# Kernel optimization log

Hardware: AMD Instinct MI355X
Metric: run time of the kernel (lower is better)

## Reference

```python
import math
import jax, jax.numpy as jnp
import numpy as np

B, FEAT, H, W = 4, 256, 48, 48
NH = 8
PE = 10            # pe_dim -> 3*PE = 30 positional channels
DK = FEAT // NH    # 32
DV = FEAT // NH    # 32
SCALE = 2.0 * math.pi
TEMPERATURE = 10000.0
BN_EPS = 1e-5


def pos_en_sine(h, w, num_pos_feats=PE):
    """3-axis sine positional encoding (y, x, and a constant 'o' axis) -> [3*PE, h, w]."""
    eps = 1e-6
    ones = jnp.ones((h, w), jnp.float32)
    y_embed = jnp.cumsum(ones, axis=0)
    x_embed = jnp.cumsum(ones, axis=1)
    y_embed = y_embed / (y_embed[-1:, :] + eps) * SCALE
    x_embed = x_embed / (x_embed[:, -1:] + eps) * SCALE
    o_embed = ones * SCALE  # third axis, constant when no explicit pos is given
    dim_t = jnp.arange(num_pos_feats, dtype=jnp.float32)
    dim_t = TEMPERATURE ** (2.0 * jnp.floor(dim_t / 2.0) / num_pos_feats)

    def enc(e):  # e: [h, w] -> [h, w, PE] interleaved sin/cos
        p = e[..., None] / dim_t
        return jnp.stack([jnp.sin(p[..., 0::2]), jnp.cos(p[..., 1::2])], axis=-1).reshape(h, w, num_pos_feats)

    pe = jnp.concatenate([enc(y_embed), enc(x_embed), enc(o_embed)], axis=-1)  # [h, w, 3*PE]
    return jnp.transpose(pe, (2, 0, 1))  # [3*PE, h, w]


def conv1x1(w, x):  # w: [out_c, in_c], x: [b, in_c, h, w]
    return jnp.einsum('oc,bchw->bohw', w, x)


def setup_inputs() -> dict:
    key = jax.random.key(0)
    ks = jax.random.split(key, 16)
    s = 0.02
    return {
        'q': jax.random.normal(ks[0], (B, FEAT, H, W), jnp.float32),
        'k': jax.random.normal(ks[1], (B, FEAT, H, W), jnp.float32),
        'v': jax.random.normal(ks[2], (B, FEAT, H, W), jnp.float32),
        'wq': jax.random.normal(ks[3], (NH * DK, FEAT + 3 * PE), jnp.float32) * s,
        'wk': jax.random.normal(ks[4], (NH * DK, FEAT + 3 * PE), jnp.float32) * s,
        'wv': jax.random.normal(ks[5], (NH * DV, FEAT), jnp.float32) * s,
        'wfc': jax.random.normal(ks[6], (FEAT, NH * DV), jnp.float32) * s,
        'w1': jax.random.normal(ks[7], (FEAT, FEAT), jnp.float32) * s,
        'b1': jnp.zeros((FEAT,), jnp.float32),
        'w2': jax.random.normal(ks[8], (FEAT, FEAT), jnp.float32) * s,
        'b2': jnp.zeros((FEAT,), jnp.float32),
        'gamma': jnp.ones((FEAT,), jnp.float32),
        'beta': jnp.zeros((FEAT,), jnp.float32),
    }


def reference(q, k, v, wq, wk, wv, wfc, w1, b1, w2, b2, gamma, beta):
    b, c, h, w = q.shape
    n = h * w
    pe = pos_en_sine(h, w)                                # [3*PE, h, w]
    peb = jnp.broadcast_to(pe[None], (b,) + pe.shape)
    qc = jnp.concatenate([q, peb], axis=1)                # [b, FEAT+30, h, w]
    kc = jnp.concatenate([k, peb], axis=1)
    # multi-head softmax attention over all spatial tokens
    Q = conv1x1(wq, qc).reshape(b, NH, DK, n)             # [b, nh, dk, n]
    K = conv1x1(wk, kc).reshape(b, NH, DK, n)
    V = conv1x1(wv, v).reshape(b, NH, DV, n)
    scores = jnp.einsum('bhdn,bhdm->bhnm', Q, K) / jnp.sqrt(jnp.float32(DK))
    attn = jax.nn.softmax(scores, axis=-1)                # [b, nh, n, n]
    O = jnp.einsum('bhnm,bhdm->bhdn', attn, V).reshape(b, NH * DV, h, w)
    O = conv1x1(wfc, O)                                   # [b, FEAT, h, w]
    # pointwise FFN + residual
    h1 = jax.nn.relu(conv1x1(w1, O) + b1[None, :, None, None])
    h2 = conv1x1(w2, h1) + b2[None, :, None, None]
    out = O + h2
    # BatchNorm2d (training mode: batch statistics over (b, h, w), biased var)
    mean = jnp.mean(out, axis=(0, 2, 3), keepdims=True)
    var = jnp.var(out, axis=(0, 2, 3), keepdims=True)
    out = (out - mean) / jnp.sqrt(var + BN_EPS)
    out = out * gamma[None, :, None, None] + beta[None, :, None, None]
    return out
```

## Files before the change

### kernel.cpp

```cpp
#include <hip/hip_runtime.h>
#include <hip/hip_bf16.h>

#define NTOK 2304

typedef short  short8  __attribute__((ext_vector_type(8)));
typedef unsigned short ushort8v __attribute__((ext_vector_type(8)));
typedef float  f32x4   __attribute__((ext_vector_type(4)));

static __device__ __forceinline__ unsigned short f2bfu(float f){
  __hip_bfloat16 h = __float2bfloat16(f);
  union { __hip_bfloat16 h; unsigned short u; } cv; cv.h = h; return cv.u;
}

static __device__ __forceinline__ void plane32(unsigned &a, unsigned &b){
  asm("v_permlane32_swap_b32 %0, %1" : "+v"(a), "+v"(b));
}
static __device__ __forceinline__ void plane16(unsigned &a, unsigned &b){
  asm("v_permlane16_swap_b32 %0, %1" : "+v"(a), "+v"(b));
}
static __device__ __forceinline__ short8 xpose_p(f32x4 sa, f32x4 sb){
  unsigned x0, x1, y0, y1;
  asm("v_cvt_pk_bf16_f32 %0, %1, %2" : "=v"(x0) : "v"(sa[0]), "v"(sa[1]));
  asm("v_cvt_pk_bf16_f32 %0, %1, %2" : "=v"(x1) : "v"(sa[2]), "v"(sa[3]));
  asm("v_cvt_pk_bf16_f32 %0, %1, %2" : "=v"(y0) : "v"(sb[0]), "v"(sb[1]));
  asm("v_cvt_pk_bf16_f32 %0, %1, %2" : "=v"(y1) : "v"(sb[2]), "v"(sb[3]));
  plane32(x0, y0);
  plane32(x1, y1);
  plane16(x0, y0);
  plane16(x1, y1);
  union { unsigned u[4]; short8 s; } r;
  r.u[0] = x0; r.u[1] = x1; r.u[2] = y0; r.u[3] = y1;
  return r.s;
}


__global__ void trip_kernel(float* out, int n){
  int i = blockIdx.x*256 + threadIdx.x;
  if (i < n) out[i] = 1000.0f;
}

__global__ __launch_bounds__(256) void setup_kernel(
    const float* __restrict__ q, const float* __restrict__ k,
    const float* __restrict__ v,
    const float* __restrict__ wq, const float* __restrict__ wk,
    const float* __restrict__ wv, const float* __restrict__ wfc,
    const float* __restrict__ w1, const float* __restrict__ w2,
    unsigned short* __restrict__ qT, unsigned short* __restrict__ kT,
    unsigned short* __restrict__ vT,
    unsigned short* __restrict__ wqp, unsigned short* __restrict__ wkp,
    unsigned short* __restrict__ wvb, unsigned short* __restrict__ wfcb,
    unsigned short* __restrict__ w1b, unsigned short* __restrict__ w2b,
    float* __restrict__ bns){
  const int bid = blockIdx.x;
  const int t = threadIdx.x;
  __shared__ __align__(16) unsigned short tile[64*72];

  if (bid < 1728){
    if (bid == 0){ bns[t] = 0.f; bns[256+t] = 0.f; }
    const int x = bid % 36, rem = bid / 36;
    const int y = rem % 4, z = rem / 4;
    const int tz = z >> 2, b = z & 3;
    const float* src = (tz==0) ? q : ((tz==1) ? k : v);
    unsigned short* dst = (tz==0) ? qT : ((tz==1) ? kT : vT);
    const int W = (tz==2) ? 256 : 288;
    const int n0 = x*64, c0 = y*64;
    const int jj = t & 7, cl = t >> 3;
    #pragma unroll
    for (int p=0; p<2; p++){
      int c = c0 + 32*p + cl;
      const float* s = src + (size_t)(b*256 + c)*NTOK + n0 + 8*jj;
      float4 f0 = *(const float4*)s;
      float4 f1 = *(const float4*)(s + 4);
      unsigned short* tr = tile + 32*p + cl;
      tr[(8*jj+0)*72] = f2bfu(f0.x); tr[(8*jj+1)*72] = f2bfu(f0.y);
      tr[(8*jj+2)*72] = f2bfu(f0.z); tr[(8*jj+3)*72] = f2bfu(f0.w);
      tr[(8*jj+4)*72] = f2bfu(f1.x); tr[(8*jj+5)*72] = f2bfu(f1.y);
      tr[(8*jj+6)*72] = f2bfu(f1.z); tr[(8*jj+7)*72] = f2bfu(f1.w);
    }
    __syncthreads();
    #pragma unroll
    for (int p=0; p<2; p++){
      int nl = 32*p + cl;
      ushort8v val = *(const ushort8v*)(tile + nl*72 + 8*jj);
      *(ushort8v*)(dst + (size_t)(b*2304 + n0 + nl)*W + c0 + 8*jj) = val;
    }
  } else if (bid < 1800){
    const int id2 = bid - 1728;
    const int x = id2 % 9, yy = id2 / 9;
    const int n = x*256 + t;
    unsigned short* buf = (yy < 4) ? qT : kT;
    const int b = yy & 3;
    const int i = n / 48, j = n - 48*i;
    const float k2pi = 6.283185307179586f;
    const float f = k2pi / 48.000001f;
    float ey = (float)(i+1) * f;
    float ex = (float)(j+1) * f;
    unsigned short u[32];
    #pragma unroll
    for (int p=0; p<10; p++){
      float inv = exp2f(-2.6575424759098898f * (float)(p >> 1));
      float vy = ey*inv, vx = ex*inv, vo = k2pi*inv;
      u[p]    = f2bfu((p&1) ? cosf(vy) : sinf(vy));
      u[10+p] = f2bfu((p&1) ? cosf(vx) : sinf(vx));
      u[20+p] = f2bfu((p&1) ? cosf(vo) : sinf(vo));
    }
    u[30] = 0; u[31] = 0;
    unsigned short* dst = buf + (size_t)(b*2304 + n)*288 + 256;
    #pragma unroll
    for (int m=0; m<4; m++) *(ushort8v*)(dst + 8*m) = *(const ushort8v*)(u + 8*m);
  } else if (bid < 2376){
    const int id3 = bid - 1800;
    const int x = id3 % 288, y = id3 / 288;
    const int idx = x*256 + t;
    const float* src = y ? wk : wq;
    unsigned short* dst = y ? wkp : wqp;
    const float scale = y ? 1.f : 0.25503486f;
    int row = idx / 288, col = idx - row*288;
    dst[idx] = (col < 286) ? f2bfu(src[row*286 + col] * scale) : (unsigned short)0;
  } else {
    const int id4 = bid - 2376;
    const int x = id4 % 256, y = id4 / 256;
    const int idx = x*256 + t;
    const float* src = (y==0)?wv:((y==1)?wfc:((y==2)?w1:w2));
    unsigned short* dst = (y==0)?wvb:((y==1)?wfcb:((y==2)?w1b:w2b));
    dst[idx] = f2bfu(src[idx]);
  }
}

template<int KSTEPS>
static __device__ __forceinline__ void gemm3_core(
    const unsigned short* __restrict__ a0,
    const unsigned short* __restrict__ a1,
    const unsigned short* __restrict__ a2,
    const unsigned short* __restrict__ wrow, int wstride, f32x4 acc[3][2]){
  #pragma unroll
  for (int kk=0; kk<KSTEPS; kk++){
    short8 af0 = *(const short8*)(a0 + 32*kk);
    short8 af1 = *(const short8*)(a1 + 32*kk);
    short8 af2 = *(const short8*)(a2 + 32*kk);
    #pragma unroll
    for (int to=0; to<2; to++){
      short8 bf = *(const short8*)(wrow + (size_t)(16*to)*wstride + 32*kk);
      acc[0][to] = __builtin_amdgcn_mfma_f32_16x16x32_bf16(af0, bf, acc[0][to], 0,0,0);
      acc[1][to] = __builtin_amdgcn_mfma_f32_16x16x32_bf16(af1, bf, acc[1][to], 0,0,0);
      acc[2][to] = __builtin_amdgcn_mfma_f32_16x16x32_bf16(af2, bf, acc[2][to], 0,0,0);
    }
  }
}

static __device__ __forceinline__ void epi_tok(
    const f32x4* acc, unsigned short* __restrict__ out_tok,
    int b, int tok, int n0, int lane, int quad, int cc,
    unsigned short* __restrict__ tlw){
  #pragma unroll
  for (int to=0; to<2; to++)
    #pragma unroll
    for (int r=0; r<4; r++)
      tlw[(4*quad + r)*40 + 16*to + cc] = f2bfu(acc[to][r]);
  const int row = lane & 15, ch = lane >> 4;
  ushort8v val = *(const ushort8v*)(tlw + row*40 + 8*ch);
  *(ushort8v*)(out_tok + (size_t)(b*2304 + tok + row)*256 + n0 + 8*ch) = val;
}

static __device__ __forceinline__ void epi_chan(
    const f32x4* acc, unsigned short* __restrict__ out_chan,
    int b, int tok, int n0, int quad, int cc){
  #pragma unroll
  for (int to=0; to<2; to++){
    ushort4 pk;
    pk.x = f2bfu(acc[to][0]); pk.y = f2bfu(acc[to][1]);
    pk.z = f2bfu(acc[to][2]); pk.w = f2bfu(acc[to][3]);
    *(ushort4*)(out_chan + (size_t)(b*256 + n0 + 16*to + cc)*NTOK + tok + 4*quad) = pk;
  }
}

__global__ __launch_bounds__(256) void qkv_kernel(
    const unsigned short* __restrict__ qT, const unsigned short* __restrict__ kT,
    const unsigned short* __restrict__ vT,
    const unsigned short* __restrict__ wqp, const unsigned short* __restrict__ wkp,
    const unsigned short* __restrict__ wvb,
    unsigned short* __restrict__ Qt, unsigned short* __restrict__ Kt,
    unsigned short* __restrict__ V2){
  const int t = threadIdx.x;
  const int w = t >> 6, lane = t & 63;
  const int quad = lane >> 4, cc = lane & 15;
  const int t0 = blockIdx.x*192, n0 = blockIdx.y*32;
  const int tz = blockIdx.z >> 2, b = blockIdx.z & 3;
  const int tok = t0 + 48*w;
  __shared__ __align__(16) unsigned short tl[4*16*40];
  unsigned short* tlw = tl + w*640;

  f32x4 acc[3][2];
  #pragma unroll
  for (int f=0; f<3; f++){
    acc[f][0] = (f32x4){0.f,0.f,0.f,0.f};
    acc[f][1] = acc[f][0];
  }

  if (tz == 0){
    const unsigned short* a0 = qT + (size_t)(b*2304 + tok + cc)*288 + 8*quad;
    gemm3_core<9>(a0, a0 + (size_t)16*288, a0 + (size_t)32*288,
                  wqp + (size_t)(n0 + cc)*288 + 8*quad, 288, acc);
    epi_tok(acc[0], Qt, b, tok,      n0, lane, quad, cc, tlw);
    epi_tok(acc[1], Qt, b, tok + 16, n0, lane, quad, cc, tlw);
    epi_tok(acc[2], Qt, b, tok + 32, n0, lane, quad, cc, tlw);
  } else if (tz == 1){
    const unsigned short* a0 = kT + (size_t)(b*2304 + tok + cc)*288 + 8*quad;
    gemm3_core<9>(a0, a0 + (size_t)16*288, a0 + (size_t)32*288,
                  wkp + (size_t)(n0 + cc)*288 + 8*quad, 288, acc);
    epi_tok(acc[0], Kt, b, tok,      n0, lane, quad, cc, tlw);
    epi_tok(acc[1], Kt, b, tok + 16, n0, lane, quad, cc, tlw);
    epi_tok(acc[2], Kt, b, tok + 32, n0, lane, quad, cc, tlw);
  } else {
    const unsigned short* a0 = vT + (size_t)(b*2304 + tok + cc)*256 + 8*quad;
    gemm3_core<8>(a0, a0 + (size_t)16*256, a0 + (size_t)32*256,
                  wvb + (size_t)(n0 + cc)*256 + 8*quad, 256, acc);
    epi_chan(acc[0], V2, b, tok,      n0, quad, cc);
    epi_chan(acc[1], V2, b, tok + 16, n0, quad, cc);
    epi_chan(acc[2], V2, b, tok + 32, n0, quad, cc);
  }
}

__global__ __launch_bounds__(256) void ffn_kernel(
    const unsigned short* __restrict__ AO,
    const unsigned short* __restrict__ wfcb,
    const unsigned short* __restrict__ w1b,
    const unsigned short* __restrict__ w2b,
    const float* __restrict__ b1, const float* __restrict__ b2,
    float* __restrict__ pre_out, float* __restrict__ bns){
  const int t = threadIdx.x;
  const int w = t >> 6, lane = t & 63;
  const int quad = lane >> 4, cc = lane & 15;
  const int tok0 = blockIdx.x * 16;
  const int b = blockIdx.y;
  const int ocb = 64 * w;

  __shared__ __align__(16) unsigned short T0[16*264];
  __shared__ __align__(16) unsigned short T1[16*264];

  const unsigned short* arow = AO + (size_t)(b*2304 + tok0 + cc)*256 + 8*quad;
  f32x4 acc1[4];
  acc1[0] = (f32x4){0.f,0.f,0.f,0.f}; acc1[1]=acc1[0]; acc1[2]=acc1[0]; acc1[3]=acc1[0];
  #pragma unroll
  for (int kk=0; kk<8; kk++){
    short8 af = *(const short8*)(arow + 32*kk);
    #pragma unroll
    for (int of=0; of<4; of++){
      short8 bf = *(const short8*)(wfcb + (size_t)(ocb + 16*of + cc)*256 + 8*quad + 32*kk);
      acc1[of] = __builtin_amdgcn_mfma_f32_16x16x32_bf16(af, bf, acc1[of], 0,0,0);
    }
  }
  #pragma unroll
  for (int of=0; of<4; of++)
    #pragma unroll
    for (int r=0; r<4; r++)
      T0[(4*quad + r)*264 + ocb + 16*of + cc] = f2bfu(acc1[of][r]);
  __syncthreads();

  f32x4 acc2[4];
  acc2[0] = (f32x4){0.f,0.f,0.f,0.f}; acc2[1]=acc2[0]; acc2[2]=acc2[0]; acc2[3]=acc2[0];
  #pragma unroll
  for (int kk=0; kk<8; kk++){
    short8 af = *(const short8*)(T0 + cc*264 + 8*quad + 32*kk);
    #pragma unroll
    for (int of=0; of<4; of++){
      short8 bf = *(const short8*)(w1b + (size_t)(ocb + 16*of + cc)*256 + 8*quad + 32*kk);
      acc2[of] = __builtin_amdgcn_mfma_f32_16x16x32_bf16(af, bf, acc2[of], 0,0,0);
    }
  }
  #pragma unroll
  for (int of=0; of<4; of++){
    float bv = b1[ocb + 16*of + cc];
    #pragma unroll
    for (int r=0; r<4; r++){
      float hv = fmaxf(acc2[of][r] + bv, 0.f);
      T1[(4*quad + r)*264 + ocb + 16*of + cc] = f2bfu(hv);
    }
  }
  __syncthreads();

  f32x4 acc3[4];
  acc3[0] = (f32x4){0.f,0.f,0.f,0.f}; acc3[1]=acc3[0]; acc3[2]=acc3[0]; acc3[3]=acc3[0];
  #pragma unroll
  for (int kk=0; kk<8; kk++){
    short8 af = *(const short8*)(T1 + cc*264 + 8*quad + 32*kk);
    #pragma unroll
    for (int of=0; of<4; of++){
      short8 bf = *(const short8*)(w2b + (size_t)(ocb + 16*of + cc)*256 + 8*quad + 32*kk);
      acc3[of] = __builtin_amdgcn_mfma_f32_16x16x32_bf16(af, bf, acc3[of], 0,0,0);
    }
  }
  #pragma unroll
  for (int of=0; of<4; of++){
    const int oc = ocb + 16*of + cc;
    float bv = b2[oc];
    float p0 = acc3[of][0] + bv + acc1[of][0];
    float p1 = acc3[of][1] + bv + acc1[of][1];
    float p2 = acc3[of][2] + bv + acc1[of][2];
    float p3 = acc3[of][3] + bv + acc1[of][3];
    *(float4*)(pre_out + (size_t)(b*256 + oc)*NTOK + tok0 + 4*quad) =
        make_float4(p0, p1, p2, p3);
    float s1 = (p0+p1)+(p2+p3);
    float s2 = (p0*p0+p1*p1)+(p2*p2+p3*p3);
    s1 += __shfl_xor(s1, 16, 64); s1 += __shfl_xor(s1, 32, 64);
    s2 += __shfl_xor(s2, 16, 64); s2 += __shfl_xor(s2, 32, 64);
    if (quad == 0){
      atomicAdd(&bns[oc],       s1);
      atomicAdd(&bns[256 + oc], s2);
    }
  }
}

__global__ __launch_bounds__(256) void attn_kernel(
    const unsigned short* __restrict__ Qt, const unsigned short* __restrict__ Kt,
    const unsigned short* __restrict__ V2, unsigned short* __restrict__ AO){
  const int t = threadIdx.x;
  const int w = t >> 6, lane = t & 63;
  const int quad = lane >> 4, cc = lane & 15;
  const int h = blockIdx.y, b = blockIdx.z;
  const int q0 = blockIdx.x*64;

  const unsigned short* qb = Qt + (size_t)(b*2304 + q0 + cc)*256 + h*32 + 8*quad;
  short8 qf0 = *(const short8*)(qb);
  short8 qf1 = *(const short8*)(qb + 16*256);
  short8 qf2 = *(const short8*)(qb + 32*256);
  short8 qf3 = *(const short8*)(qb + 48*256);

  const unsigned short* kb = Kt + (size_t)(b*2304 + cc)*256 + h*32 + 8*quad;
  const unsigned short* vb = V2 + (size_t)(b*256 + h*32 + cc)*NTOK + 8*quad;

  __shared__ __align__(16) float mg_lds[4*1600];

  f32x4 o00={0.f,0.f,0.f,0.f}, o10=o00, o01=o00, o11=o00;
  f32x4 o02=o00, o12=o00, o03=o00, o13=o00;
  float lsum0=0.f, lsum1=0.f, lsum2=0.f, lsum3=0.f;

  const int kstart = w*576;
  short8 kf0 = *(const short8*)(kb + (size_t)kstart*256);
  short8 kf1 = *(const short8*)(kb + (size_t)(kstart+16)*256);
  short8 vf0 = *(const short8*)(vb + kstart);
  short8 vf1 = *(const short8*)(vb + (size_t)16*NTOK + kstart);

  #pragma unroll 1
  for (int it = 0; it < 18; ++it){
    const int ko = kstart + it*32;
    const int rk = (it < 17) ? ko + 32 : kstart;
    const f32x4 z = {0.f,0.f,0.f,0.f};

    f32x4 s00 = __builtin_amdgcn_mfma_f32_16x16x32_bf16(kf0, qf0, z, 0,0,0);
    f32x4 s10 = __builtin_amdgcn_mfma_f32_16x16x32_bf16(kf1, qf0, z, 0,0,0);
    f32x4 s01 = __builtin_amdgcn_mfma_f32_16x16x32_bf16(kf0, qf1, z, 0,0,0);
    f32x4 s11 = __builtin_amdgcn_mfma_f32_16x16x32_bf16(kf1, qf1, z, 0,0,0);
    f32x4 s02 = __builtin_amdgcn_mfma_f32_16x16x32_bf16(kf0, qf2, z, 0,0,0);
    f32x4 s12 = __builtin_amdgcn_mfma_f32_16x16x32_bf16(kf1, qf2, z, 0,0,0);
    f32x4 s03 = __builtin_amdgcn_mfma_f32_16x16x32_bf16(kf0, qf3, z, 0,0,0);
    f32x4 s13 = __builtin_amdgcn_mfma_f32_16x16x32_bf16(kf1, qf3, z, 0,0,0);
    kf0 = *(const short8*)(kb + (size_t)rk*256);
    kf1 = *(const short8*)(kb + (size_t)(rk+16)*256);

    #pragma unroll
    for (int r=0; r<4; r++){
      s00[r] = __builtin_amdgcn_exp2f(s00[r]);
      s10[r] = __builtin_amdgcn_exp2f(s10[r]);
      s01[r] = __builtin_amdgcn_exp2f(s01[r]);
      s11[r] = __builtin_amdgcn_exp2f(s11[r]);
      s02[r] = __builtin_amdgcn_exp2f(s02[r]);
      s12[r] = __builtin_amdgcn_exp2f(s12[r]);
      s03[r] = __builtin_amdgcn_exp2f(s03[r]);
      s13[r] = __builtin_amdgcn_exp2f(s13[r]);
    }
    lsum0 += ((s00[0]+s00[1])+(s00[2]+s00[3])) + ((s10[0]+s10[1])+(s10[2]+s10[3]));
    lsum1 += ((s01[0]+s01[1])+(s01[2]+s01[3])) + ((s11[0]+s11[1])+(s11[2]+s11[3]));
    lsum2 += ((s02[0]+s02[1])+(s02[2]+s02[3])) + ((s12[0]+s12[1])+(s12[2]+s12[3]));
    lsum3 += ((s03[0]+s03[1])+(s03[2]+s03[3])) + ((s13[0]+s13[1])+(s13[2]+s13[3]));

    short8 pf0 = xpose_p(s00, s10);
    short8 pf1 = xpose_p(s01, s11);
    short8 pf2 = xpose_p(s02, s12);
    short8 pf3 = xpose_p(s03, s13);

    o00 = __builtin_amdgcn_mfma_f32_16x16x32_bf16(vf0, pf0, o00, 0,0,0);
    o10 = __builtin_amdgcn_mfma_f32_16x16x32_bf16(vf1, pf0, o10, 0,0,0);
    o01 = __builtin_amdgcn_mfma_f32_16x16x32_bf16(vf0, pf1, o01, 0,0,0);
    o11 = __builtin_amdgcn_mfma_f32_16x16x32_bf16(vf1, pf1, o11, 0,0,0);
    o02 = __builtin_amdgcn_mfma_f32_16x16x32_bf16(vf0, pf2, o02, 0,0,0);
    o12 = __builtin_amdgcn_mfma_f32_16x16x32_bf16(vf1, pf2, o12, 0,0,0);
    o03 = __builtin_amdgcn_mfma_f32_16x16x32_bf16(vf0, pf3, o03, 0,0,0);
    o13 = __builtin_amdgcn_mfma_f32_16x16x32_bf16(vf1, pf3, o13, 0,0,0);
    vf0 = *(const short8*)(vb + rk);
    vf1 = *(const short8*)(vb + (size_t)16*NTOK + rk);
  }

  lsum0 += __shfl_xor(lsum0, 16, 64); lsum0 += __shfl_xor(lsum0, 32, 64);
  lsum1 += __shfl_xor(lsum1, 16, 64); lsum1 += __shfl_xor(lsum1, 32, 64);
  lsum2 += __shfl_xor(lsum2, 16, 64); lsum2 += __shfl_xor(lsum2, 32, 64);
  lsum3 += __shfl_xor(lsum3, 16, 64); lsum3 += __shfl_xor(lsum3, 32, 64);

  float* mg = mg_lds + w*1600;
  #pragma unroll
  for (int qq=0; qq<4; qq++){
    f32x4 a0, a1;
    if (qq==0){ a0=o00; a1=o10; }
    else if (qq==1){ a0=o01; a1=o11; }
    else if (qq==2){ a0=o02; a1=o12; }
    else { a0=o03; a1=o13; }
    if (qq != w){
      const int p = (qq < w) ? qq : qq - 1;
      #pragma unroll
      for (int i=0;i<4;i++){
        mg[(p*8 + i)*64 + lane]     = a0[i];
        mg[(p*8 + 4 + i)*64 + lane] = a1[i];
      }
    }
  }
  if (quad == 0){
    mg[1536 +  0 + cc] = lsum0;
    mg[1536 + 16 + cc] = lsum1;
    mg[1536 + 32 + cc] = lsum2;
    mg[1536 + 48 + cc] = lsum3;
  }
  __syncthreads();

  f32x4 R0, R1; float ls;
  if (w==0){ R0=o00; R1=o10; ls=lsum0; }
  else if (w==1){ R0=o01; R1=o11; ls=lsum1; }
  else if (w==2){ R0=o02; R1=o12; ls=lsum2; }
  else { R0=o03; R1=o13; ls=lsum3; }
  #pragma unroll
  for (int v=0; v<4; v++){
    if (v == w) continue;
    const float* m = mg_lds + v*1600;
    const int p = (w < v) ? w : w - 1;
    #pragma unroll
    for (int i=0;i<4;i++){
      R0[i] += m[(p*8 + i)*64 + lane];
      R1[i] += m[(p*8 + 4 + i)*64 + lane];
    }
    ls += m[1536 + w*16 + cc];
  }
  float inv = 1.f / ls;

  const int qcol = q0 + w*16 + cc;
  unsigned short* dst = AO + (size_t)(b*2304 + qcol)*256 + h*32 + 4*quad;
  ushort4 p0;
  p0.x = f2bfu(R0[0]*inv); p0.y = f2bfu(R0[1]*inv);
  p0.z = f2bfu(R0[2]*inv); p0.w = f2bfu(R0[3]*inv);
  *(ushort4*)(dst) = p0;
  ushort4 p1;
  p1.x = f2bfu(R1[0]*inv); p1.y = f2bfu(R1[1]*inv);
  p1.z = f2bfu(R1[2]*inv); p1.w = f2bfu(R1[3]*inv);
  *(ushort4*)(dst + 16) = p1;
}

__global__ __launch_bounds__(256) void bn_final_kernel(
    const float* __restrict__ pre, const float* __restrict__ bns,
    const float* __restrict__ g, const float* __restrict__ bt,
    float* __restrict__ out){
  int i0 = (blockIdx.x*256 + threadIdx.x)*4;
  int ch = (i0 / NTOK) & 255;
  float mean = bns[ch] * (1.f/9216.f);
  float var  = bns[256+ch] * (1.f/9216.f) - mean*mean;
  float scl = g[ch] * rsqrtf(fmaxf(var, 0.f) + 1e-5f);
  float sh  = bt[ch] - mean*scl;
  float4 x = *(const float4*)(pre + i0);
  *(float4*)(out + i0) = make_float4(x.x*scl+sh, x.y*scl+sh, x.z*scl+sh, x.w*scl+sh);
}

extern "C" void kernel_launch(void* const* d_in, const int* in_sizes, int n_in,
                              void* d_out, int out_size, void* d_ws, size_t ws_size,
                              hipStream_t stream){
  const size_t NEED = 2112 + (size_t)15155200*2;
  if (ws_size < NEED){
    trip_kernel<<<dim3((out_size+255)/256), dim3(256), 0, stream>>>((float*)d_out, out_size);
    return;
  }
  const float* q   = (const float*)d_in[0];
  const float* k   = (const float*)d_in[1];
  const float* v   = (const float*)d_in[2];
  const float* wq  = (const float*)d_in[3];
  const float* wk  = (const float*)d_in[4];
  const float* wv  = (const float*)d_in[5];
  const float* wfc = (const float*)d_in[6];
  const float* w1  = (const float*)d_in[7];
  const float* b1  = (const float*)d_in[8];
  const float* w2  = (const float*)d_in[9];
  const float* b2  = (const float*)d_in[10];
  const float* gm  = (const float*)d_in[11];
  const float* bt  = (const float*)d_in[12];

  float* ws  = (float*)d_ws;
  float* bns = ws;
  unsigned short* ub = (unsigned short*)(ws + 528);
  unsigned short* u_qT = ub;
  unsigned short* u_kT = ub + 2654208;
  unsigned short* u_vT = ub + 5308416;
  unsigned short* u_Qt = ub + 7667712;
  unsigned short* u_Kt = ub + 10027008;
  unsigned short* u_V2 = ub + 12386304;
  unsigned short* wqp  = ub + 14745600;
  unsigned short* wkp  = ub + 14819328;
  unsigned short* wvb  = ub + 14893056;
  unsigned short* wfcb = ub + 14958592;
  unsigned short* w1b  = ub + 15024128;
  unsigned short* w2b  = ub + 15089664;
  unsigned short* AO  = u_qT;
  float* pre = (float*)(u_Kt);

  setup_kernel<<<dim3(3400), dim3(256), 0, stream>>>(
      q, k, v, wq, wk, wv, wfc, w1, w2,
      u_qT, u_kT, u_vT, wqp, wkp, wvb, wfcb, w1b, w2b, bns);

  qkv_kernel<<<dim3(12,8,12), dim3(256), 0, stream>>>(u_qT, u_kT, u_vT, wqp, wkp, wvb, u_Qt, u_Kt, u_V2);

  attn_kernel<<<dim3(36,8,4), dim3(256), 0, stream>>>(u_Qt, u_Kt, u_V2, AO);

  ffn_kernel<<<dim3(144,4), dim3(256), 0, stream>>>(AO, wfcb, w1b, w2b, b1, b2, pre, bns);

  bn_final_kernel<<<dim3(2304), dim3(256), 0, stream>>>(pre, bns, gm, bt, (float*)d_out);
}
```

Before: 220.8 us.

## Fuse BatchNorm finalization into FFN kernel via grid-wide atomic barrier

Removes the separate bn_final kernel and the fp32 pre-normalization intermediate buffer. Each FFN block keeps its results in registers, increments a global counter and spins until all 576 blocks have contributed their channel statistics. It then reads the reduced sums and writes normalized output directly. This saves a full write and read of the activation tensor plus one launch. The cost is a spin barrier that only works if every block is co-resident, which should hold for 576 blocks on this GPU.

```diff
diff --git a/kernel.cpp b/kernel.cpp
--- a/kernel.cpp
+++ b/kernel.cpp
@@ -56,7 +56,10 @@
   __shared__ __align__(16) unsigned short tile[64*72];
 
   if (bid < 1728){
-    if (bid == 0){ bns[t] = 0.f; bns[256+t] = 0.f; }
+    if (bid == 0){
+      bns[t] = 0.f; bns[256+t] = 0.f;
+      if (t == 0) *(unsigned*)(bns + 512) = 0u;
+    }
     const int x = bid % 36, rem = bid / 36;
     const int y = rem % 4, z = rem / 4;
     const int tz = z >> 2, b = z & 3;
@@ -227,7 +230,9 @@
     const unsigned short* __restrict__ w1b,
     const unsigned short* __restrict__ w2b,
     const float* __restrict__ b1, const float* __restrict__ b2,
-    float* __restrict__ pre_out, float* __restrict__ bns){
+    const float* __restrict__ gm, const float* __restrict__ bt,
+    float* __restrict__ out, float* __restrict__ bns,
+    unsigned* __restrict__ ctr){
   const int t = threadIdx.x;
   const int w = t >> 6, lane = t & 63;
   const int quad = lane >> 4, cc = lane & 15;
@@ -298,8 +303,6 @@
     float p1 = acc3[of][1] + bv + acc1[of][1];
     float p2 = acc3[of][2] + bv + acc1[of][2];
     float p3 = acc3[of][3] + bv + acc1[of][3];
-    *(float4*)(pre_out + (size_t)(b*256 + oc)*NTOK + tok0 + 4*quad) =
-        make_float4(p0, p1, p2, p3);
     float s1 = (p0+p1)+(p2+p3);
     float s2 = (p0*p0+p1*p1)+(p2*p2+p3*p3);
     s1 += __shfl_xor(s1, 16, 64); s1 += __shfl_xor(s1, 32, 64);
@@ -308,6 +311,33 @@
       atomicAdd(&bns[oc],       s1);
       atomicAdd(&bns[256 + oc], s2);
     }
+  }
+
+  __threadfence();
+  __syncthreads();
+  if (t == 0){
+    atomicAdd(ctr, 1u);
+    const unsigned nb = gridDim.x * gridDim.y;
+    while (atomicAdd(ctr, 0u) < nb){ __builtin_amdgcn_s_sleep(2); }
+  }
+  __syncthreads();
+
+  #pragma unroll
+  for (int of=0; of<4; of++){
+    const int oc = ocb + 16*of + cc;
+    float sA = atomicAdd(&bns[oc],       0.f);
+    float sB = atomicAdd(&bns[256 + oc], 0.f);
+    float mean = sA * (1.f/9216.f);
+    float var  = sB * (1.f/9216.f) - mean*mean;
+    float scl = gm[oc] * rsqrtf(fmaxf(var, 0.f) + 1e-5f);
+    float sh  = bt[oc] - mean*scl;
+    float bv = b2[oc];
+    float p0 = acc3[of][0] + bv + acc1[of][0];
+    float p1 = acc3[of][1] + bv + acc1[of][1];
+    float p2 = acc3[of][2] + bv + acc1[of][2];
+    float p3 = acc3[of][3] + bv + acc1[of][3];
+    *(float4*)(out + (size_t)(b*256 + oc)*NTOK + tok0 + 4*quad) =
+        make_float4(p0*scl+sh, p1*scl+sh, p2*scl+sh, p3*scl+sh);
   }
 }
 
@@ -452,20 +482,6 @@
   *(ushort4*)(dst + 16) = p1;
 }
 
-__global__ __launch_bounds__(256) void bn_final_kernel(
-    const float* __restrict__ pre, const float* __restrict__ bns,
-    const float* __restrict__ g, const float* __restrict__ bt,
-    float* __restrict__ out){
-  int i0 = (blockIdx.x*256 + threadIdx.x)*4;
-  int ch = (i0 / NTOK) & 255;
-  float mean = bns[ch] * (1.f/9216.f);
-  float var  = bns[256+ch] * (1.f/9216.f) - mean*mean;
-  float scl = g[ch] * rsqrtf(fmaxf(var, 0.f) + 1e-5f);
-  float sh  = bt[ch] - mean*scl;
-  float4 x = *(const float4*)(pre + i0);
-  *(float4*)(out + i0) = make_float4(x.x*scl+sh, x.y*scl+sh, x.z*scl+sh, x.w*scl+sh);
-}
-
 extern "C" void kernel_launch(void* const* d_in, const int* in_sizes, int n_in,
                               void* d_out, int out_size, void* d_ws, size_t ws_size,
                               hipStream_t stream){
@@ -490,6 +506,7 @@
 
   float* ws  = (float*)d_ws;
   float* bns = ws;
+  unsigned* ctr = (unsigned*)(ws + 512);
   unsigned short* ub = (unsigned short*)(ws + 528);
   unsigned short* u_qT = ub;
   unsigned short* u_kT = ub + 2654208;
@@ -504,7 +521,6 @@
   unsigned short* w1b  = ub + 15024128;
   unsigned short* w2b  = ub + 15089664;
   unsigned short* AO  = u_qT;
-  float* pre = (float*)(u_Kt);
 
   setup_kernel<<<dim3(3400), dim3(256), 0, stream>>>(
       q, k, v, wq, wk, wv, wfc, w1, w2,
@@ -514,7 +530,6 @@
 
   attn_kernel<<<dim3(36,8,4), dim3(256), 0, stream>>>(u_Qt, u_Kt, u_V2, AO);
 
-  ffn_kernel<<<dim3(144,4), dim3(256), 0, stream>>>(AO, wfcb, w1b, w2b, b1, b2, pre, bns);
-
-  bn_final_kernel<<<dim3(2304), dim3(256), 0, stream>>>(pre, bns, gm, bt, (float*)d_out);
-}
+  ffn_kernel<<<dim3(144,4), dim3(256), 0, stream>>>(
+      AO, wfcb, w1b, w2b, b1, b2, gm, bt, (float*)d_out, bns, ctr);
+}
```

Result: slower. 587.0 us (+165.8%).
